# Kernel optimization log

Measured on AMD Instinct MI355X. Metric: run time of the kernel, lower is better.

Reference implementation:

```python
import jax, jax.numpy as jnp
import numpy as np

B, IN, OUT, LUT_SIZE = 32, 8192, 16384, 256


def setup_inputs() -> dict:
    key = jax.random.key(0)
    k1, k2, k3 = jax.random.split(key, 3)
    x = jax.random.normal(k1, (B, IN), dtype=jnp.float32)
    # int8 weight codes, stored as indices in [0, 256) into the dequant LUT
    weight_idx = jax.random.randint(k2, (OUT, IN), 0, LUT_SIZE, dtype=jnp.int32)
    # symmetric uniform dequant levels: code c -> (c - 128) * scale
    scale = jnp.float32(0.05 / 128.0)
    lut = (jnp.arange(LUT_SIZE, dtype=jnp.float32) - 128.0) * scale  # [256]
    bias = jax.random.normal(k3, (OUT,), dtype=jnp.float32) * 0.02
    return {"x": x, "lut": lut, "bias": bias, "weight_idx": weight_idx}


def reference(x, lut, bias, weight_idx):
    # LUT dequantization: gather fp32 weight values from the 256-entry table
    W = lut[weight_idx]                      # [OUT, IN] fp32
    # y = x @ W^T + b   (einsum: b=batch tokens, i=in_features, o=out_features)
    return jnp.einsum("bi,oi->bo", x, W) + bias  # [B, OUT]
```

## Files before the change

kernel.cpp:

```cpp
#include <hip/hip_runtime.h>

#define IN_F   8192
#define OUT_F  16384
#define BATCH  32
#define NWAVE  8
#define KSLICE (IN_F / NWAVE)

typedef __attribute__((ext_vector_type(8))) short  bf16x8;
typedef __attribute__((ext_vector_type(4))) float  f32x4;

__device__ __forceinline__ unsigned f2bf(float f) {
    unsigned u = __builtin_bit_cast(unsigned, f);
    return (u + 0x7fffu + ((u >> 16) & 1u)) >> 16;
}

__device__ __forceinline__ unsigned pk_i2bf(int a, int b) {
    unsigned fa = __builtin_bit_cast(unsigned, (float)a);
    unsigned fb = __builtin_bit_cast(unsigned, (float)b);
#if __has_builtin(__builtin_amdgcn_perm)
    return __builtin_amdgcn_perm(fb, fa, 0x07060302u);
#else
    return (fa >> 16) | (fb & 0xffff0000u);
#endif
}

__global__ __launch_bounds__(256) void prep_kernel(
        const float* __restrict__ x, const float* __restrict__ lut,
        unsigned short* __restrict__ xbf, float* __restrict__ sumx) {
    const int b = blockIdx.x;
    const int t = threadIdx.x;
    const float s = lut[129];
    const float4* xr = (const float4*)(x + b * IN_F);
    ushort4* xo = (ushort4*)(xbf + b * IN_F);
    float acc = 0.f;
    #pragma unroll
    for (int i = 0; i < IN_F / 4 / 256; ++i) {
        float4 v = xr[t + i * 256];
        acc += v.x + v.y + v.z + v.w;
        ushort4 o;
        o.x = (unsigned short)f2bf(v.x * s);
        o.y = (unsigned short)f2bf(v.y * s);
        o.z = (unsigned short)f2bf(v.z * s);
        o.w = (unsigned short)f2bf(v.w * s);
        xo[t + i * 256] = o;
    }
    __shared__ float red[256];
    red[t] = acc;
    __syncthreads();
    for (int off = 128; off > 0; off >>= 1) {
        if (t < off) red[t] += red[t + off];
        __syncthreads();
    }
    if (t == 0) sumx[b] = red[0];
}

__global__ __launch_bounds__(512, 6) void gemm_kernel(
        const unsigned short* __restrict__ xbf,
        const int* __restrict__ widx,
        const float* __restrict__ bias,
        const float* __restrict__ lut,
        const float* __restrict__ sumx,
        float* __restrict__ out) {
    __shared__ float part[NWAVE * 512];

    const int tid   = threadIdx.x;
    const int wave  = tid >> 6;
    const int lane  = tid & 63;
    const int col16 = lane & 15;
    const int quad  = lane >> 4;
    const int ntile = blockIdx.x;
    const int n     = ntile * 16 + col16;
    const int k0    = wave * KSLICE + quad * 8;

    const int* wp = widx + (long)n * IN_F + k0;
    const unsigned short* xp0 = xbf + col16 * IN_F + k0;
    const unsigned short* xp1 = xp0 + 16 * IN_F;

    f32x4 acc0 = {0.f, 0.f, 0.f, 0.f};
    f32x4 acc1 = {0.f, 0.f, 0.f, 0.f};

    int4   c0 = *(const int4*)wp;
    int4   c1 = *(const int4*)(wp + 4);
    bf16x8 a0 = *(const bf16x8*)xp0;
    bf16x8 a1 = *(const bf16x8*)xp1;

    #pragma unroll 2
    for (int kk = 32; kk < KSLICE; kk += 32) {
        int4   p0 = *(const int4*)(wp + kk);
        int4   p1 = *(const int4*)(wp + kk + 4);
        bf16x8 q0 = *(const bf16x8*)(xp0 + kk);
        bf16x8 q1 = *(const bf16x8*)(xp1 + kk);

        union { unsigned u[4]; bf16x8 v; } bB;
        bB.u[0] = pk_i2bf(c0.x, c0.y);
        bB.u[1] = pk_i2bf(c0.z, c0.w);
        bB.u[2] = pk_i2bf(c1.x, c1.y);
        bB.u[3] = pk_i2bf(c1.z, c1.w);
        acc0 = __builtin_amdgcn_mfma_f32_16x16x32_bf16(a0, bB.v, acc0, 0, 0, 0);
        acc1 = __builtin_amdgcn_mfma_f32_16x16x32_bf16(a1, bB.v, acc1, 0, 0, 0);

        c0 = p0; c1 = p1; a0 = q0; a1 = q1;
    }
    {
        union { unsigned u[4]; bf16x8 v; } bB;
        bB.u[0] = pk_i2bf(c0.x, c0.y);
        bB.u[1] = pk_i2bf(c0.z, c0.w);
        bB.u[2] = pk_i2bf(c1.x, c1.y);
        bB.u[3] = pk_i2bf(c1.z, c1.w);
        acc0 = __builtin_amdgcn_mfma_f32_16x16x32_bf16(a0, bB.v, acc0, 0, 0, 0);
        acc1 = __builtin_amdgcn_mfma_f32_16x16x32_bf16(a1, bB.v, acc1, 0, 0, 0);
    }

    #pragma unroll
    for (int r = 0; r < 4; ++r) {
        part[wave * 512 + (quad * 4 + r) * 16 + col16]        = acc0[r];
        part[wave * 512 + (quad * 4 + r + 16) * 16 + col16]   = acc1[r];
    }
    __syncthreads();

    {
        const int m = tid >> 4, nn = tid & 15;
        float ssum = 0.f;
        #pragma unroll
        for (int w = 0; w < NWAVE; ++w) ssum += part[w * 512 + tid];
        float o = bias[ntile * 16 + nn] + lut[0] * sumx[m] + ssum;
        out[(long)m * OUT_F + ntile * 16 + nn] = o;
    }
}

extern "C" void kernel_launch(void* const* d_in, const int* in_sizes, int n_in,
                              void* d_out, int out_size, void* d_ws, size_t ws_size,
                              hipStream_t stream) {
    const float* x    = (const float*)d_in[0];
    const float* lut  = (const float*)d_in[1];
    const float* bias = (const float*)d_in[2];
    const int*   widx = (const int*)d_in[3];
    float* out = (float*)d_out;

    unsigned short* xbf = (unsigned short*)d_ws;
    float* sumx = (float*)((char*)d_ws + BATCH * IN_F * 2);

    prep_kernel<<<BATCH, 256, 0, stream>>>(x, lut, xbf, sumx);
    gemm_kernel<<<OUT_F / 16, 512, 0, stream>>>(xbf, widx, bias, lut, sumx, out);
}
```

Baseline: 741.3 us.

## Stage weight-index tiles through LDS with coalesced row loads per K chunk

Rewrites the GEMM main loop to load 16x512 chunks of int32 weight codes with fully coalesced row-contiguous 16-byte loads into padded LDS, then has each wave read its MFMA B fragments from LDS. Block size drops from 8 waves to 4 waves, each covering a quarter of each chunk, and the partial-sum reduction shrinks to match. The goal is better DRAM coalescing than the previous per-lane strided row reads. In exchange it adds two barriers per chunk with no double buffering, so load latency is no longer hidden by register prefetch.

```diff
diff --git a/kernel.cpp b/kernel.cpp
--- a/kernel.cpp
+++ b/kernel.cpp
@@ -3,8 +3,9 @@
 #define IN_F   8192
 #define OUT_F  16384
 #define BATCH  32
-#define NWAVE  8
-#define KSLICE (IN_F / NWAVE)
+#define KC     512
+#define NCHUNK (IN_F / KC)
+#define LDSS   516
 
 typedef __attribute__((ext_vector_type(8))) short  bf16x8;
 typedef __attribute__((ext_vector_type(4))) float  f32x4;
@@ -54,14 +55,14 @@
     if (t == 0) sumx[b] = red[0];
 }
 
-__global__ __launch_bounds__(512, 6) void gemm_kernel(
+__global__ __launch_bounds__(256, 4) void gemm_kernel(
         const unsigned short* __restrict__ xbf,
         const int* __restrict__ widx,
         const float* __restrict__ bias,
         const float* __restrict__ lut,
         const float* __restrict__ sumx,
         float* __restrict__ out) {
-    __shared__ float part[NWAVE * 512];
+    __shared__ int lds[16 * LDSS];
 
     const int tid   = threadIdx.x;
     const int wave  = tid >> 6;
@@ -69,62 +70,70 @@
     const int col16 = lane & 15;
     const int quad  = lane >> 4;
     const int ntile = blockIdx.x;
-    const int n     = ntile * 16 + col16;
-    const int k0    = wave * KSLICE + quad * 8;
 
-    const int* wp = widx + (long)n * IN_F + k0;
-    const unsigned short* xp0 = xbf + col16 * IN_F + k0;
+    const int  srow  = wave * 4;
+    const long gbase = (long)(ntile * 16) * IN_F;
+    const int  kw    = wave * (KC / 4);
+
+    const unsigned short* xp0 = xbf + col16 * IN_F + quad * 8;
     const unsigned short* xp1 = xp0 + 16 * IN_F;
 
     f32x4 acc0 = {0.f, 0.f, 0.f, 0.f};
     f32x4 acc1 = {0.f, 0.f, 0.f, 0.f};
 
-    int4   c0 = *(const int4*)wp;
-    int4   c1 = *(const int4*)(wp + 4);
-    bf16x8 a0 = *(const bf16x8*)xp0;
-    bf16x8 a1 = *(const bf16x8*)xp1;
+    for (int ch = 0; ch < NCHUNK; ++ch) {
+        const int kbase = ch * KC;
 
-    #pragma unroll 2
-    for (int kk = 32; kk < KSLICE; kk += 32) {
-        int4   p0 = *(const int4*)(wp + kk);
-        int4   p1 = *(const int4*)(wp + kk + 4);
-        bf16x8 q0 = *(const bf16x8*)(xp0 + kk);
-        bf16x8 q1 = *(const bf16x8*)(xp1 + kk);
+        int4 st[8];
+        #pragma unroll
+        for (int i = 0; i < 8; ++i) {
+            const int r   = srow + (i >> 1);
+            const int off = (i & 1) * 256;
+            st[i] = *(const int4*)(widx + gbase + (long)r * IN_F + kbase + off + lane * 4);
+        }
+        __syncthreads();
+        #pragma unroll
+        for (int i = 0; i < 8; ++i) {
+            const int r   = srow + (i >> 1);
+            const int off = (i & 1) * 256;
+            *(int4*)&lds[r * LDSS + off + lane * 4] = st[i];
+        }
+        __syncthreads();
 
-        union { unsigned u[4]; bf16x8 v; } bB;
-        bB.u[0] = pk_i2bf(c0.x, c0.y);
-        bB.u[1] = pk_i2bf(c0.z, c0.w);
-        bB.u[2] = pk_i2bf(c1.x, c1.y);
-        bB.u[3] = pk_i2bf(c1.z, c1.w);
-        acc0 = __builtin_amdgcn_mfma_f32_16x16x32_bf16(a0, bB.v, acc0, 0, 0, 0);
-        acc1 = __builtin_amdgcn_mfma_f32_16x16x32_bf16(a1, bB.v, acc1, 0, 0, 0);
+        #pragma unroll
+        for (int kk = 0; kk < KC / 4; kk += 32) {
+            const int kl = kw + kk;
+            int4 c0 = *(const int4*)&lds[col16 * LDSS + kl + quad * 8];
+            int4 c1 = *(const int4*)&lds[col16 * LDSS + kl + quad * 8 + 4];
+            bf16x8 a0 = *(const bf16x8*)(xp0 + kbase + kl);
+            bf16x8 a1 = *(const bf16x8*)(xp1 + kbase + kl);
 
-        c0 = p0; c1 = p1; a0 = q0; a1 = q1;
-    }
-    {
-        union { unsigned u[4]; bf16x8 v; } bB;
-        bB.u[0] = pk_i2bf(c0.x, c0.y);
-        bB.u[1] = pk_i2bf(c0.z, c0.w);
-        bB.u[2] = pk_i2bf(c1.x, c1.y);
-        bB.u[3] = pk_i2bf(c1.z, c1.w);
-        acc0 = __builtin_amdgcn_mfma_f32_16x16x32_bf16(a0, bB.v, acc0, 0, 0, 0);
-        acc1 = __builtin_amdgcn_mfma_f32_16x16x32_bf16(a1, bB.v, acc1, 0, 0, 0);
+            union { unsigned u[4]; bf16x8 v; } bB;
+            bB.u[0] = pk_i2bf(c0.x, c0.y);
+            bB.u[1] = pk_i2bf(c0.z, c0.w);
+            bB.u[2] = pk_i2bf(c1.x, c1.y);
+            bB.u[3] = pk_i2bf(c1.z, c1.w);
+            acc0 = __builtin_amdgcn_mfma_f32_16x16x32_bf16(a0, bB.v, acc0, 0, 0, 0);
+            acc1 = __builtin_amdgcn_mfma_f32_16x16x32_bf16(a1, bB.v, acc1, 0, 0, 0);
+        }
     }
 
+    __syncthreads();
+    float* fp = (float*)lds;
     #pragma unroll
     for (int r = 0; r < 4; ++r) {
-        part[wave * 512 + (quad * 4 + r) * 16 + col16]        = acc0[r];
-        part[wave * 512 + (quad * 4 + r + 16) * 16 + col16]   = acc1[r];
+        fp[wave * 512 + (quad * 4 + r) * 16 + col16]      = acc0[r];
+        fp[wave * 512 + (quad * 4 + r + 16) * 16 + col16] = acc1[r];
     }
     __syncthreads();
 
-    {
-        const int m = tid >> 4, nn = tid & 15;
-        float ssum = 0.f;
-        #pragma unroll
-        for (int w = 0; w < NWAVE; ++w) ssum += part[w * 512 + tid];
-        float o = bias[ntile * 16 + nn] + lut[0] * sumx[m] + ssum;
-        out[(long)m * OUT_F + ntile * 16 + nn] = o;
+    const float lut0 = lut[0];
+    #pragma unroll
+    for (int e = tid; e < 512; e += 256) {
+        const int m = e >> 4, nn = e & 15;
+        float ssum = fp[e] + fp[512 + e] + fp[1024 + e] + fp[1536 + e];
+        out[(long)m * OUT_F + ntile * 16 + nn] =
+            bias[ntile * 16 + nn] + lut0 * sumx[m] + ssum;
     }
 }
 
@@ -141,5 +150,5 @@
     float* sumx = (float*)((char*)d_ws + BATCH * IN_F * 2);
 
     prep_kernel<<<BATCH, 256, 0, stream>>>(x, lut, xbf, sumx);
-    gemm_kernel<<<OUT_F / 16, 512, 0, stream>>>(xbf, widx, bias, lut, sumx, out);
+    gemm_kernel<<<OUT_F / 16, 256, 0, stream>>>(xbf, widx, bias, lut, sumx, out);
 }
```

Measured after the change: 789.2 us. 6.5% more time.
